# Kernel optimization log

Measured on AMD Instinct MI355X. Metric: run time of the kernel, lower is better.

Reference implementation:

```python
import jax
import jax.numpy as jnp
import numpy as np

IN_FEATS = 784
HIDDEN_DIM = 1024
BATCH = 1024


def setup_inputs() -> dict:
    key = jax.random.key(0)
    k_px, k_W, k_c, k_V, k_b = jax.random.split(key, 5)
    pixels = jax.random.uniform(k_px, (BATCH, IN_FEATS), dtype=jnp.float32)
    W = jax.random.normal(k_W, (HIDDEN_DIM, IN_FEATS), dtype=jnp.float32)
    c = jax.random.normal(k_c, (HIDDEN_DIM,), dtype=jnp.float32)
    V = jax.random.normal(k_V, (IN_FEATS, HIDDEN_DIM), dtype=jnp.float32)
    b = jax.random.normal(k_b, (IN_FEATS,), dtype=jnp.float32)
    return {"pixels": pixels, "W": W, "c": c, "V": V, "b": b}


def reference(pixels, W, c, V, b):
    # pixels: [B, D]; W: [H, D]; c: [H]; V: [D, H]; b: [D]
    B = pixels.shape[0]
    a0 = jnp.broadcast_to(c[None, :], (B, c.shape[0]))  # [B, H]

    def step(a, inp):
        w_col, v_row, b_i, x_i = inp  # [H], [H], [], [B]
        h = jax.nn.sigmoid(a)                     # [B, H]
        pred_i = b_i + h @ v_row                  # [B]
        a_next = a + w_col[None, :] * x_i[:, None]  # rank-1 accumulator update
        return a_next, pred_i

    xs = (W.T, V, b, pixels.T)  # each leading dim D (scan over visible units)
    _, preds = jax.lax.scan(step, a0, xs)  # preds: [D, B]
    return preds.T  # [B, D]
```

## Files before the change

### kernel.cpp

```cpp
#include <hip/hip_runtime.h>

#define B_ 1024
#define D_ 784
#define H_ 1024
#define BH_ (B_ * H_)
#define LOG2E 1.4426950408889634f


__device__ __forceinline__ int seg_bound(int s) {
    const int b[7] = {0, 132, 264, 396, 528, 656, 784};
    return b[s];
}

__global__ __launch_bounds__(256) void prep(const float* __restrict__ V,
                                            const float* __restrict__ W,
                                            const float* __restrict__ px,
                                            float* __restrict__ VW,
                                            float* __restrict__ G) {
    __shared__ float smem[32 * 33];
    const int t = threadIdx.x;

    if (blockIdx.x < 800) {
        int i0 = (blockIdx.x % 25) * 32;
        int h0 = (blockIdx.x / 25) * 32;
        int tx = t & 31, ty = t >> 5;
        int hb = h0 >> 8, hl = h0 & 255;
#pragma unroll
        for (int j = 0; j < 4; ++j) {
            int i = i0 + ty + j * 8;
            if (i < D_)
                VW[((size_t)i * 4 + hb) * 512 + hl + tx] = V[(size_t)i * H_ + h0 + tx];
        }
#pragma unroll
        for (int j = 0; j < 4; ++j) {
            int h = h0 + ty + j * 8;
            int i = i0 + tx;
            float v = 0.f;
            if (i < D_) v = W[(size_t)h * D_ + i] * LOG2E;
            smem[(ty + j * 8) * 33 + tx] = v;
        }
        __syncthreads();
#pragma unroll
        for (int j = 0; j < 4; ++j) {
            int i = i0 + ty + j * 8;
            if (i < D_)
                VW[((size_t)i * 4 + hb) * 512 + 256 + hl + tx] = smem[tx * 33 + ty + j * 8];
        }
    } else {
        float* xs = smem;
        float* ws = smem + 256;
        int idx = blockIdx.x - 800;
        int r   = idx >> 8;
        int b0  = (idx & 15) * 64;
        int h0  = ((idx >> 4) & 15) * 64;
        int j0s = seg_bound(r), j1s = seg_bound(r + 1);

        const int tb = t >> 4, th = t & 15;
        float acc[4][4];
#pragma unroll
        for (int bi = 0; bi < 4; ++bi)
#pragma unroll
            for (int hh = 0; hh < 4; ++hh) acc[bi][hh] = 0.f;

        for (int j0 = j0s; j0 < j1s; j0 += 4) {
            float xv = px[(size_t)(b0 + (t >> 2)) * D_ + j0 + (t & 3)];
            float4 wv = make_float4(0, 0, 0, 0);
            if (t < 64) wv = *(const float4*)(W + (size_t)(h0 + t) * D_ + j0);
            __syncthreads();
            xs[(t & 3) * 64 + (t >> 2)] = xv;
            if (t < 64) {
                ws[0 * 64 + t] = wv.x * LOG2E;
                ws[1 * 64 + t] = wv.y * LOG2E;
                ws[2 * 64 + t] = wv.z * LOG2E;
                ws[3 * 64 + t] = wv.w * LOG2E;
            }
            __syncthreads();
#pragma unroll
            for (int jj = 0; jj < 4; ++jj) {
                float4 xb = *(float4*)&xs[jj * 64 + tb * 4];
                float4 wb = *(float4*)&ws[jj * 64 + th * 4];
                float xa[4] = {xb.x, xb.y, xb.z, xb.w};
                float wa[4] = {wb.x, wb.y, wb.z, wb.w};
#pragma unroll
                for (int bi = 0; bi < 4; ++bi)
#pragma unroll
                    for (int hh = 0; hh < 4; ++hh)
                        acc[bi][hh] = fmaf(xa[bi], wa[hh], acc[bi][hh]);
            }
        }
        float* dst = G + (size_t)r * BH_;
#pragma unroll
        for (int bi = 0; bi < 4; ++bi) {
            float4 o = make_float4(acc[bi][0], acc[bi][1], acc[bi][2], acc[bi][3]);
            *(float4*)(dst + (size_t)(b0 + tb * 4 + bi) * H_ + h0 + th * 4) = o;
        }
    }
}

template <int CTRL>
__device__ __forceinline__ float dpp_add(float p) {
    int s = __builtin_amdgcn_update_dpp(0, __float_as_int(p), CTRL, 0xf, 0xf, true);
    return p + __int_as_float(s);
}
__device__ __forceinline__ float reduce_halves(float p) {
    p = dpp_add<0x111>(p);
    p = dpp_add<0x112>(p);
    p = dpp_add<0x114>(p);
    p = dpp_add<0x118>(p);
    p = dpp_add<0x142>(p);
    return p;
}

__global__ __launch_bounds__(256, 6) void nade_main(
    const float* __restrict__ px,
    const float* __restrict__ c,
    const float* __restrict__ VW,
    const float* __restrict__ G,
    float* __restrict__ part)
{
    const int lane = threadIdx.x & 63;
    const int wid  = threadIdx.x >> 6;
    const int gw   = blockIdx.x * 4 + wid;
    const int s    = gw % 6;
    const int r4   = gw / 6;
    const int hb   = r4 & 3;
    const int rp   = r4 >> 2;
    const int half = lane >> 5;
    const int row  = rp * 2 + half;
    const int hl   = lane & 31;
    const int h0   = hb * 256 + hl * 8;

    const int i0s = seg_bound(s), i1s = seg_bound(s + 1);

    float A[8];
    {
        float4 c0 = *(const float4*)(c + h0);
        float4 c1 = *(const float4*)(c + h0 + 4);
        A[0] = c0.x * LOG2E; A[1] = c0.y * LOG2E; A[2] = c0.z * LOG2E; A[3] = c0.w * LOG2E;
        A[4] = c1.x * LOG2E; A[5] = c1.y * LOG2E; A[6] = c1.z * LOG2E; A[7] = c1.w * LOG2E;
        for (int r = 0; r < s; ++r) {
            const float* gp = G + (size_t)r * BH_ + (size_t)row * H_ + h0;
            float4 g0 = *(const float4*)(gp);
            float4 g1 = *(const float4*)(gp + 4);
            A[0] += g0.x; A[1] += g0.y; A[2] += g0.z; A[3] += g0.w;
            A[4] += g1.x; A[5] += g1.y; A[6] += g1.z; A[7] += g1.w;
        }
    }

    const float* xp = px + (size_t)row * D_;
    float*       pp = part + ((size_t)hb * B_ + row) * D_;
    const float* vw = VW + ((size_t)i0s * 4 + hb) * 512 + hl * 8;

    auto step8 = [&A](const float4& v0, const float4& v1,
                      const float4& w0, const float4& w1, float xi) -> float {
        float va[8] = {v0.x, v0.y, v0.z, v0.w, v1.x, v1.y, v1.z, v1.w};
        float wa[8] = {w0.x, w0.y, w0.z, w0.w, w1.x, w1.y, w1.z, w1.w};
        float q[8];
#pragma unroll
        for (int k = 0; k < 8; ++k) {
            float e = __builtin_amdgcn_exp2f(fminf(15.f, -A[k]));
            q[k] = 1.f + e;
            A[k] = fmaf(wa[k], xi, A[k]);
        }
        float a01 = fmaf(va[0], q[1], va[1] * q[0]);
        float a23 = fmaf(va[2], q[3], va[3] * q[2]);
        float a45 = fmaf(va[4], q[5], va[5] * q[4]);
        float a67 = fmaf(va[6], q[7], va[7] * q[6]);
        float q01 = q[0] * q[1], q23 = q[2] * q[3];
        float q45 = q[4] * q[5], q67 = q[6] * q[7];
        float n0123 = fmaf(a01, q23, a23 * q01);
        float n4567 = fmaf(a45, q67, a67 * q45);
        float q0123 = q01 * q23, q4567 = q45 * q67;
        float r = __builtin_amdgcn_rcpf(q0123 * q4567);
        float n = fmaf(n0123, q4567, n4567 * q0123);
        return n * r;
    };

    float4 v0 = *(const float4*)(vw + 0),   v1 = *(const float4*)(vw + 4);
    float4 w0 = *(const float4*)(vw + 256), w1 = *(const float4*)(vw + 260);
    vw += 2048;
    float4 xq = *(const float4*)(xp + i0s);

    for (int ib = i0s; ib < i1s; ib += 4) {
        int xb = (ib + 4 < i1s) ? (ib + 4) : i0s;
        float4 xq_n = *(const float4*)(xp + xb);
        float xa[4] = {xq.x, xq.y, xq.z, xq.w};
        float pr[4];
#pragma unroll
        for (int j = 0; j < 4; ++j) {
            float4 v0n = *(const float4*)(vw + 0),   v1n = *(const float4*)(vw + 4);
            float4 w0n = *(const float4*)(vw + 256), w1n = *(const float4*)(vw + 260);
            vw += 2048;
            float p = step8(v0, v1, w0, w1, xa[j]);
            pr[j] = reduce_halves(p);
            v0 = v0n; v1 = v1n; w0 = w0n; w1 = w1n;
        }
        if (hl == 31) *(float4*)(pp + ib) = make_float4(pr[0], pr[1], pr[2], pr[3]);
        xq = xq_n;
    }
}

__global__ __launch_bounds__(256) void reduce_out(const float* __restrict__ part,
                                                  const float* __restrict__ bias,
                                                  float* __restrict__ out) {
    int t = blockIdx.x * 256 + threadIdx.x;
    if (t >= B_ * (D_ / 4)) return;
    int row = t / (D_ / 4);
    int ic  = (t - row * (D_ / 4)) * 4;
    float4 acc = *(const float4*)(bias + ic);
    const float* p = part + (size_t)row * D_ + ic;
#pragma unroll
    for (int hb = 0; hb < 4; ++hb) {
        float4 v = *(const float4*)(p + (size_t)hb * B_ * D_);
        acc.x += v.x; acc.y += v.y; acc.z += v.z; acc.w += v.w;
    }
    *(float4*)(out + (size_t)row * D_ + ic) = acc;
}

extern "C" void kernel_launch(void* const* d_in, const int* in_sizes, int n_in,
                              void* d_out, int out_size, void* d_ws, size_t ws_size,
                              hipStream_t stream) {
    const float* px   = (const float*)d_in[0];
    const float* W    = (const float*)d_in[1];
    const float* c    = (const float*)d_in[2];
    const float* V    = (const float*)d_in[3];
    const float* bias = (const float*)d_in[4];
    float* out = (float*)d_out;

    float* VW   = (float*)d_ws;
    float* G    = VW + (size_t)788 * 2048;
    float* part = G + (size_t)5 * BH_;

    prep<<<dim3(2080), 256, 0, stream>>>(V, W, px, VW, G);

    nade_main<<<dim3(3072), 256, 0, stream>>>(px, c, VW, G, part);

    reduce_out<<<dim3((B_ * (D_ / 4) + 255) / 256), 256, 0, stream>>>(part, bias, out);
}
```

Before: 319.9 us.

## Stage VW rows through LDS with async global_load_lds and packed-math exp2

Each block now shares one segment and head-block across its four waves, which cooperatively stream V/W rows into a triple-buffered LDS ring using global_load_lds instead of every wave loading them from global memory directly. The VW layout is re-swizzled so lanes read conflict-free float4s from LDS. The hardware exp2 is replaced by a software polynomial exp2 built on packed FP32 FMA instructions, and the accumulator update also uses packed math. In exchange it adds a per-chunk __syncthreads, LDS pressure that may limit occupancy, and extra VALU work for the polynomial.

```diff
diff --git a/kernel.cpp b/kernel.cpp
--- a/kernel.cpp
+++ b/kernel.cpp
@@ -1,4 +1,5 @@
 #include <hip/hip_runtime.h>
+#include <stdint.h>
 
 #define B_ 1024
 #define D_ 784
@@ -7,15 +8,51 @@
 #define LOG2E 1.4426950408889634f
 
 
+typedef float v2f __attribute__((ext_vector_type(2)));
+
+__device__ __forceinline__ v2f pk_fma(v2f a, v2f b, v2f c) {
+    v2f d; asm("v_pk_fma_f32 %0, %1, %2, %3" : "=v"(d) : "v"(a), "v"(b), "v"(c)); return d;
+}
+__device__ __forceinline__ v2f pk_add(v2f a, v2f b) {
+    v2f d; asm("v_pk_add_f32 %0, %1, %2" : "=v"(d) : "v"(a), "v"(b)); return d;
+}
+__device__ __forceinline__ v2f pk_sub(v2f a, v2f b) {
+    v2f d; asm("v_pk_add_f32 %0, %1, %2 neg_lo:[0,1] neg_hi:[0,1]" : "=v"(d) : "v"(a), "v"(b)); return d;
+}
+__device__ __forceinline__ v2f pk_mul(v2f a, v2f b) {
+    v2f d; asm("v_pk_mul_f32 %0, %1, %2" : "=v"(d) : "v"(a), "v"(b)); return d;
+}
+
+__device__ __forceinline__ v2f exp2_pk(v2f t) {
+    const v2f MG = {12582912.f, 12582912.f};
+    v2f m = pk_add(t, MG);
+    v2f n = pk_sub(m, MG);
+    v2f f = pk_sub(t, n);
+    v2f p = {0.0013333558f, 0.0013333558f};
+    p = pk_fma(p, f, (v2f){0.0096181291f, 0.0096181291f});
+    p = pk_fma(p, f, (v2f){0.0555041087f, 0.0555041087f});
+    p = pk_fma(p, f, (v2f){0.2402265070f, 0.2402265070f});
+    p = pk_fma(p, f, (v2f){0.6931471806f, 0.6931471806f});
+    p = pk_fma(p, f, (v2f){1.0f, 1.0f});
+    v2f s;
+    s.x = __uint_as_float((__float_as_uint(m.x) << 23) + 0x3F800000u);
+    s.y = __uint_as_float((__float_as_uint(m.y) << 23) + 0x3F800000u);
+    return pk_mul(s, p);
+}
+
 __device__ __forceinline__ int seg_bound(int s) {
     const int b[7] = {0, 132, 264, 396, 528, 656, 784};
     return b[s];
 }
 
+__device__ __forceinline__ size_t vw_idx(int i, int h) {
+    return ((size_t)i * 4 + (h >> 8)) * 512 + ((h >> 2) & 1) * 128 + (((h & 255) >> 3) * 4) + (h & 3);
+}
+
 __global__ __launch_bounds__(256) void prep(const float* __restrict__ V,
                                             const float* __restrict__ W,
                                             const float* __restrict__ px,
-                                            float* __restrict__ VW,
+                                            float* __restrict__ VWs,
                                             float* __restrict__ G) {
     __shared__ float smem[32 * 33];
     const int t = threadIdx.x;
@@ -24,12 +61,11 @@
         int i0 = (blockIdx.x % 25) * 32;
         int h0 = (blockIdx.x / 25) * 32;
         int tx = t & 31, ty = t >> 5;
-        int hb = h0 >> 8, hl = h0 & 255;
 #pragma unroll
         for (int j = 0; j < 4; ++j) {
             int i = i0 + ty + j * 8;
-            if (i < D_)
-                VW[((size_t)i * 4 + hb) * 512 + hl + tx] = V[(size_t)i * H_ + h0 + tx];
+            int h = h0 + tx;
+            if (i < D_) VWs[vw_idx(i, h)] = V[(size_t)i * H_ + h];
         }
 #pragma unroll
         for (int j = 0; j < 4; ++j) {
@@ -43,8 +79,8 @@
 #pragma unroll
         for (int j = 0; j < 4; ++j) {
             int i = i0 + ty + j * 8;
-            if (i < D_)
-                VW[((size_t)i * 4 + hb) * 512 + 256 + hl + tx] = smem[tx * 33 + ty + j * 8];
+            int h = h0 + tx;
+            if (i < D_) VWs[vw_idx(i, h) + 256] = smem[tx * 33 + ty + j * 8];
         }
     } else {
         float* xs = smem;
@@ -114,60 +150,84 @@
 __global__ __launch_bounds__(256, 6) void nade_main(
     const float* __restrict__ px,
     const float* __restrict__ c,
-    const float* __restrict__ VW,
+    const float* __restrict__ VWs,
     const float* __restrict__ G,
     float* __restrict__ part)
 {
+    __shared__ float lds[3 * 2048];
+
     const int lane = threadIdx.x & 63;
     const int wid  = threadIdx.x >> 6;
-    const int gw   = blockIdx.x * 4 + wid;
-    const int s    = gw % 6;
-    const int r4   = gw / 6;
-    const int hb   = r4 & 3;
-    const int rp   = r4 >> 2;
+    const int bid  = blockIdx.x;
+    const int s    = bid % 6;
+    const int t2   = bid / 6;
+    const int hb   = t2 & 3;
+    const int rpg  = t2 >> 2;
     const int half = lane >> 5;
-    const int row  = rp * 2 + half;
     const int hl   = lane & 31;
+    const int row  = rpg * 8 + wid * 2 + half;
     const int h0   = hb * 256 + hl * 8;
 
     const int i0s = seg_bound(s), i1s = seg_bound(s + 1);
-
-    float A[8];
+    const int nchunk = (i1s - i0s) >> 2;
+
+    v2f A01, A23, A45, A67;
     {
         float4 c0 = *(const float4*)(c + h0);
         float4 c1 = *(const float4*)(c + h0 + 4);
-        A[0] = c0.x * LOG2E; A[1] = c0.y * LOG2E; A[2] = c0.z * LOG2E; A[3] = c0.w * LOG2E;
-        A[4] = c1.x * LOG2E; A[5] = c1.y * LOG2E; A[6] = c1.z * LOG2E; A[7] = c1.w * LOG2E;
+        A01 = (v2f){c0.x * LOG2E, c0.y * LOG2E};
+        A23 = (v2f){c0.z * LOG2E, c0.w * LOG2E};
+        A45 = (v2f){c1.x * LOG2E, c1.y * LOG2E};
+        A67 = (v2f){c1.z * LOG2E, c1.w * LOG2E};
         for (int r = 0; r < s; ++r) {
             const float* gp = G + (size_t)r * BH_ + (size_t)row * H_ + h0;
             float4 g0 = *(const float4*)(gp);
             float4 g1 = *(const float4*)(gp + 4);
-            A[0] += g0.x; A[1] += g0.y; A[2] += g0.z; A[3] += g0.w;
-            A[4] += g1.x; A[5] += g1.y; A[6] += g1.z; A[7] += g1.w;
+            A01 = pk_add(A01, (v2f){g0.x, g0.y});
+            A23 = pk_add(A23, (v2f){g0.z, g0.w});
+            A45 = pk_add(A45, (v2f){g1.x, g1.y});
+            A67 = pk_add(A67, (v2f){g1.z, g1.w});
         }
     }
 
     const float* xp = px + (size_t)row * D_;
     float*       pp = part + ((size_t)hb * B_ + row) * D_;
-    const float* vw = VW + ((size_t)i0s * 4 + hb) * 512 + hl * 8;
-
-    auto step8 = [&A](const float4& v0, const float4& v1,
-                      const float4& w0, const float4& w1, float xi) -> float {
-        float va[8] = {v0.x, v0.y, v0.z, v0.w, v1.x, v1.y, v1.z, v1.w};
-        float wa[8] = {w0.x, w0.y, w0.z, w0.w, w1.x, w1.y, w1.z, w1.w};
-        float q[8];
-#pragma unroll
-        for (int k = 0; k < 8; ++k) {
-            float e = __builtin_amdgcn_exp2f(fminf(15.f, -A[k]));
-            q[k] = 1.f + e;
-            A[k] = fmaf(wa[k], xi, A[k]);
-        }
-        float a01 = fmaf(va[0], q[1], va[1] * q[0]);
-        float a23 = fmaf(va[2], q[3], va[3] * q[2]);
-        float a45 = fmaf(va[4], q[5], va[5] * q[4]);
-        float a67 = fmaf(va[6], q[7], va[7] * q[6]);
-        float q01 = q[0] * q[1], q23 = q[2] * q[3];
-        float q45 = q[4] * q[5], q67 = q[6] * q[7];
+
+    auto stage = [&](int step, int bufidx) {
+        const float* src = VWs + (((size_t)step * 4 + hb) << 9) + lane * 4;
+        float* dst = &lds[bufidx * 2048 + wid * 512 + lane * 4];
+        __builtin_amdgcn_global_load_lds((__attribute__((address_space(1))) void*)(src),
+                                         (__attribute__((address_space(3))) void*)(dst), 16, 0, 0);
+        __builtin_amdgcn_global_load_lds((__attribute__((address_space(1))) void*)(src + 256),
+                                         (__attribute__((address_space(3))) void*)(dst + 256), 16, 0, 0);
+    };
+
+    auto step8 = [&](float4 v0f, float4 v1f, float4 w0f, float4 w1f, float xi) -> float {
+        v2f t0, t1, t2, t3;
+        t0.x = __builtin_amdgcn_fmed3f(-A01.x, -126.f, 15.f);
+        t0.y = __builtin_amdgcn_fmed3f(-A01.y, -126.f, 15.f);
+        t1.x = __builtin_amdgcn_fmed3f(-A23.x, -126.f, 15.f);
+        t1.y = __builtin_amdgcn_fmed3f(-A23.y, -126.f, 15.f);
+        t2.x = __builtin_amdgcn_fmed3f(-A45.x, -126.f, 15.f);
+        t2.y = __builtin_amdgcn_fmed3f(-A45.y, -126.f, 15.f);
+        t3.x = __builtin_amdgcn_fmed3f(-A67.x, -126.f, 15.f);
+        t3.y = __builtin_amdgcn_fmed3f(-A67.y, -126.f, 15.f);
+        v2f one = {1.f, 1.f};
+        v2f q0 = pk_add(exp2_pk(t0), one);
+        v2f q1 = pk_add(exp2_pk(t1), one);
+        v2f q2 = pk_add(exp2_pk(t2), one);
+        v2f q3 = pk_add(exp2_pk(t3), one);
+        v2f xx = {xi, xi};
+        A01 = pk_fma((v2f){w0f.x, w0f.y}, xx, A01);
+        A23 = pk_fma((v2f){w0f.z, w0f.w}, xx, A23);
+        A45 = pk_fma((v2f){w1f.x, w1f.y}, xx, A45);
+        A67 = pk_fma((v2f){w1f.z, w1f.w}, xx, A67);
+        float a01 = fmaf(v0f.x, q0.y, v0f.y * q0.x);
+        float a23 = fmaf(v0f.z, q1.y, v0f.w * q1.x);
+        float a45 = fmaf(v1f.x, q2.y, v1f.y * q2.x);
+        float a67 = fmaf(v1f.z, q3.y, v1f.w * q3.x);
+        float q01 = q0.x * q0.y, q23 = q1.x * q1.y;
+        float q45 = q2.x * q2.y, q67 = q3.x * q3.y;
         float n0123 = fmaf(a01, q23, a23 * q01);
         float n4567 = fmaf(a45, q67, a67 * q45);
         float q0123 = q01 * q23, q4567 = q45 * q67;
@@ -176,27 +236,32 @@
         return n * r;
     };
 
-    float4 v0 = *(const float4*)(vw + 0),   v1 = *(const float4*)(vw + 4);
-    float4 w0 = *(const float4*)(vw + 256), w1 = *(const float4*)(vw + 260);
-    vw += 2048;
+    stage(i0s + wid, 0);
+    stage(i0s + 4 + wid, 1);
+    __syncthreads();
+
     float4 xq = *(const float4*)(xp + i0s);
 
-    for (int ib = i0s; ib < i1s; ib += 4) {
-        int xb = (ib + 4 < i1s) ? (ib + 4) : i0s;
-        float4 xq_n = *(const float4*)(xp + xb);
+    for (int ck = 0; ck < nchunk; ++ck) {
+        const int ib = i0s + ck * 4;
+        if (ck + 2 < nchunk) stage(ib + 8 + wid, (ck + 2) % 3);
+        float4 xq_n = (ck + 1 < nchunk) ? *(const float4*)(xp + ib + 4) : xq;
+
+        const float* bufp = &lds[(ck % 3) * 2048 + hl * 4];
         float xa[4] = {xq.x, xq.y, xq.z, xq.w};
         float pr[4];
 #pragma unroll
         for (int j = 0; j < 4; ++j) {
-            float4 v0n = *(const float4*)(vw + 0),   v1n = *(const float4*)(vw + 4);
-            float4 w0n = *(const float4*)(vw + 256), w1n = *(const float4*)(vw + 260);
-            vw += 2048;
-            float p = step8(v0, v1, w0, w1, xa[j]);
-            pr[j] = reduce_halves(p);
-            v0 = v0n; v1 = v1n; w0 = w0n; w1 = w1n;
+            const float* base = bufp + j * 512;
+            float4 v0 = *(const float4*)(base);
+            float4 v1 = *(const float4*)(base + 128);
+            float4 w0 = *(const float4*)(base + 256);
+            float4 w1 = *(const float4*)(base + 384);
+            pr[j] = reduce_halves(step8(v0, v1, w0, w1, xa[j]));
         }
         if (hl == 31) *(float4*)(pp + ib) = make_float4(pr[0], pr[1], pr[2], pr[3]);
         xq = xq_n;
+        __syncthreads();
     }
 }
 
@@ -227,13 +292,13 @@
     const float* bias = (const float*)d_in[4];
     float* out = (float*)d_out;
 
-    float* VW   = (float*)d_ws;
-    float* G    = VW + (size_t)788 * 2048;
+    float* VWs  = (float*)d_ws;
+    float* G    = VWs + (size_t)792 * 2048;
     float* part = G + (size_t)5 * BH_;
 
-    prep<<<dim3(2080), 256, 0, stream>>>(V, W, px, VW, G);
-
-    nade_main<<<dim3(3072), 256, 0, stream>>>(px, c, VW, G, part);
+    prep<<<dim3(2080), 256, 0, stream>>>(V, W, px, VWs, G);
+
+    nade_main<<<dim3(3072), 256, 0, stream>>>(px, c, VWs, G, part);
 
     reduce_out<<<dim3((B_ * (D_ / 4) + 255) / 256), 256, 0, stream>>>(part, bias, out);
 }
```

Measured after the change: 424.4 us. 1.33x slower.
